# Kernel optimization log

Hardware: AMD Instinct MI355X
Metric: run time of the kernel (lower is better)

## Reference

```python
import jax, jax.numpy as jnp
import numpy as np

B, S, H, NH = 1, 4096, 768, 12
D = H // NH  # per-head dim = 64


def setup_inputs() -> dict:
    key = jax.random.key(0)
    ks = jax.random.split(key, 10)
    p = 0.02  # param scale
    return {
        "x": jax.random.normal(ks[0], (B, S, H), jnp.float32),
        "Wq": jax.random.normal(ks[1], (H, H), jnp.float32) * p,
        "bq": jax.random.normal(ks[2], (H,), jnp.float32) * p,
        "Wk": jax.random.normal(ks[3], (H, H), jnp.float32) * p,
        "bk": jax.random.normal(ks[4], (H,), jnp.float32) * p,
        "Wv": jax.random.normal(ks[5], (H, H), jnp.float32) * p,
        "bv": jax.random.normal(ks[6], (H,), jnp.float32) * p,
        "Wo": jax.random.normal(ks[7], (H, H), jnp.float32) * p,
        "bo": jax.random.normal(ks[8], (H,), jnp.float32) * p,
        "attn_mask": jax.random.randint(ks[9], (B, 1, 1, S), 0, 2).astype(bool),
    }


def _split_heads(t):
    # [B, S, H] -> [B, NH, S, D]
    return t.reshape(B, S, NH, D).transpose(0, 2, 1, 3)


def reference(x, Wq, bq, Wk, bk, Wv, bv, Wo, bo, attn_mask):
    q = _split_heads(x @ Wq.T + bq)
    k = _split_heads(x @ Wk.T + bk)
    v = _split_heads(x @ Wv.T + bv)
    scores = jnp.einsum('bhqd,bhkd->bhqk', q, k) / np.sqrt(D).astype(np.float32)
    scores = jnp.where(attn_mask, jnp.float32(-1e9), scores)
    attn = jax.nn.softmax(scores, axis=-1)
    ctx = jnp.einsum('bhqk,bhkd->bhqd', attn, v)
    ctx = ctx.transpose(0, 2, 1, 3).reshape(B, S, H)  # merge heads
    return ctx @ Wo.T + bo
```

## Files before the change

### kernel.cpp

```cpp
#include <hip/hip_runtime.h>
#include <stdint.h>

#define S_LEN 4096
#define HDIM  768
#define NHEAD 12
#define DHEAD 64

typedef _Float16 f16;
typedef __attribute__((ext_vector_type(8)))  _Float16 f16x8;
typedef __attribute__((ext_vector_type(4)))  _Float16 f16x4;
typedef __attribute__((ext_vector_type(4)))  float    f32x4;
typedef __attribute__((ext_vector_type(16))) float    f32x16;

typedef __attribute__((address_space(1))) void gv_t;
typedef __attribute__((address_space(3))) void lv_t;

__device__ __forceinline__ void async_copy16(const void* g, void* l) {
  __builtin_amdgcn_global_load_lds((gv_t*)g, (lv_t*)l, 16, 0, 0);
}

__device__ __forceinline__ float fast_exp2(float x) {
#if __has_builtin(__builtin_amdgcn_exp2f)
  return __builtin_amdgcn_exp2f(x);
#else
  return exp2f(x);
#endif
}

__device__ __forceinline__ int swz4(int row) { return (row ^ (row >> 2)) & 3; }

constexpr size_t OFF_META = 0;
constexpr size_t OFF_RIDX = 256;
constexpr size_t OFF_XB   = 65536;
constexpr size_t SZ_XB    = (size_t)S_LEN * HDIM * 2;
constexpr size_t OFF_WQKV = OFF_XB + SZ_XB;
constexpr size_t SZ_WQKV  = (size_t)3 * HDIM * HDIM * 2;
constexpr size_t OFF_WO   = OFF_WQKV + SZ_WQKV;
constexpr size_t SZ_WO    = (size_t)HDIM * HDIM * 2;
constexpr size_t OFF_Q    = OFF_WO + SZ_WO;
constexpr size_t SZ_HD    = (size_t)NHEAD * S_LEN * DHEAD * 2;
constexpr size_t OFF_K    = OFF_Q + SZ_HD;
constexpr size_t OFF_VT   = OFF_K + SZ_HD;
constexpr size_t OFF_PO   = OFF_VT + SZ_HD;

__global__ __launch_bounds__(256) void k_prep(const float* __restrict__ x,
                                              const float* __restrict__ wq,
                                              const float* __restrict__ wk,
                                              const float* __restrict__ wv,
                                              const float* __restrict__ wo,
                                              const int* __restrict__ mi,
                                              f16* __restrict__ dst,
                                              int* __restrict__ ridx,
                                              int* __restrict__ meta) {
  __shared__ int s_flag;
  __shared__ int s_cnt[256];
  const int b = blockIdx.x, tid = threadIdx.x;
  if (b < 5376) {
    int i = b * 256 + tid;
    const float* src; int off;
    if (i < 786432) { src = x; off = i; }
    else {
      int j = i - 786432;
      int w = j / 147456;
      off = j - w * 147456;
      src = (w == 0) ? wq : (w == 1) ? wk : (w == 2) ? wv : wo;
    }
    float4 v = ((const float4*)src)[off];
    f16x4 h;
    h[0] = (f16)v.x; h[1] = (f16)v.y; h[2] = (f16)v.z; h[3] = (f16)v.w;
    ((f16x4*)dst)[i] = h;
    return;
  }
  if (tid == 0) s_flag = 1;
  __syncthreads();
  int bad = 0;
  #pragma unroll
  for (int k = 0; k < 4; ++k) {
    int v = mi[k * 256 + tid];
    if (v != 0 && v != 1) bad = 1;
  }
  if (bad) atomicAnd(&s_flag, 0);
  __syncthreads();
  const int isInt = s_flag;
  const unsigned char* mu8 = (const unsigned char*)mi;
  int keep[16]; int cnt = 0;
  const int s0 = tid * 16;
  #pragma unroll
  for (int k = 0; k < 16; ++k) {
    int mval = isInt ? mi[s0 + k] : (int)mu8[s0 + k];
    keep[k] = (mval == 0) ? 1 : 0;
    cnt += keep[k];
    ridx[s0 + k] = 0;
  }
  s_cnt[tid] = cnt;
  __syncthreads();
  for (int off = 1; off < 256; off <<= 1) {
    int t = (tid >= off) ? s_cnt[tid - off] : 0;
    __syncthreads();
    s_cnt[tid] += t;
    __syncthreads();
  }
  int base = s_cnt[tid] - cnt;
  #pragma unroll
  for (int k = 0; k < 16; ++k) {
    if (keep[k]) { ridx[base] = s0 + k; ++base; }
  }
  if (tid == 255) meta[0] = s_cnt[255];
}

__global__ __launch_bounds__(256) void k_qkv(
    const f16* __restrict__ xb, const f16* __restrict__ wqkv,
    const float* __restrict__ bq, const float* __restrict__ bk, const float* __restrict__ bv,
    const int* __restrict__ ridx, const int* __restrict__ meta,
    f16* __restrict__ Qh, f16* __restrict__ Kc, f16* __restrict__ Vtc) {
  __shared__ __attribute__((aligned(16))) f16 lA[128 * 64];
  __shared__ __attribute__((aligned(16))) f16 lB[128 * 64];
  __shared__ __attribute__((aligned(16))) f16 lT[64 * 132];
  const int tid = threadIdx.x;
  const int wid = tid >> 6, lane = tid & 63;
  const int hf = lane >> 5, l31 = lane & 31;
  const int wm = wid >> 1, wn = wid & 1;
  const int tn = blockIdx.x;
  const int m0 = blockIdx.y * 128;
  const int mat = tn / 6;
  const int nb = (tn % 6) * 128;
  const int kc = meta[0];
  const int kcp = (kc + 63) & ~63;
  if (mat != 0 && m0 >= kc) return;
  const f16* wbase = wqkv + (size_t)mat * HDIM * HDIM;

  const int r8 = tid >> 3;
  const int slot = tid & 7;
  const int gs = slot ^ (r8 & 7);
  const f16* asrc[4];
  #pragma unroll
  for (int it = 0; it < 4; ++it) {
    int r = it * 32 + r8;
    if (mat == 0) {
      asrc[it] = xb + (size_t)(m0 + r) * HDIM;
    } else {
      int g = (m0 + r < kc) ? ridx[m0 + r] : 0;
      asrc[it] = xb + (size_t)g * HDIM;
    }
  }

  f32x16 acc[2][2] = {};

  for (int k0 = 0; k0 < HDIM; k0 += 64) {
    #pragma unroll
    for (int it = 0; it < 4; ++it) {
      int r = it * 32 + r8;
      async_copy16((const char*)(asrc[it] + k0) + gs * 16,
                   (char*)lA + (it * 256 + wid * 64) * 16);
      async_copy16((const char*)(wbase + (size_t)(nb + r) * HDIM + k0) + gs * 16,
                   (char*)lB + (it * 256 + wid * 64) * 16);
    }
    __syncthreads();
    #pragma unroll
    for (int kk = 0; kk < 4; ++kk) {
      f16x8 af[2], bf[2];
      #pragma unroll
      for (int mi = 0; mi < 2; ++mi) {
        int row = wm * 64 + mi * 32 + l31;
        af[mi] = *(const f16x8*)&lA[row * 64 + ((((kk << 1) | hf) ^ (row & 7)) * 8)];
      }
      #pragma unroll
      for (int ni = 0; ni < 2; ++ni) {
        int row = wn * 64 + ni * 32 + l31;
        bf[ni] = *(const f16x8*)&lB[row * 64 + ((((kk << 1) | hf) ^ (row & 7)) * 8)];
      }
      #pragma unroll
      for (int mi = 0; mi < 2; ++mi)
        #pragma unroll
        for (int ni = 0; ni < 2; ++ni)
          acc[mi][ni] = __builtin_amdgcn_mfma_f32_32x32x16_f16(af[mi], bf[ni], acc[mi][ni], 0, 0, 0);
    }
    __syncthreads();
  }

  if (mat == 2) {
    const float* bias = bv;
    #pragma unroll
    for (int pass = 0; pass < 2; ++pass) {
      __syncthreads();
      if (wn == pass) {
        #pragma unroll
        for (int ni = 0; ni < 2; ++ni) {
          const int n = nb + wn * 64 + ni * 32 + l31;
          const float bn = bias[n];
          const int dloc = ni * 32 + l31;
          #pragma unroll
          for (int mi = 0; mi < 2; ++mi) {
            #pragma unroll
            for (int rg = 0; rg < 4; ++rg) {
              const int sbase = wm * 64 + mi * 32 + 8 * rg + 4 * hf;
              f16x4 v4;
              #pragma unroll
              for (int j = 0; j < 4; ++j) {
                const int s = m0 + sbase + j;
                v4[j] = (s < kc) ? (f16)(acc[mi][ni][rg * 4 + j] + bn) : (f16)0.f;
              }
              *(f16x4*)&lT[dloc * 132 + sbase] = v4;
            }
          }
        }
      }
      __syncthreads();
      const int headg = (nb >> 6) + pass;
      for (int u2 = tid; u2 < 1024; u2 += 256) {
        const int d = u2 >> 4, p8 = u2 & 15;
        const int base16 = (p8 >> 1) * 16, half = p8 & 1;
        f16x4 lo = *(const f16x4*)&lT[d * 132 + base16 + half * 4];
        f16x4 hi = *(const f16x4*)&lT[d * 132 + base16 + 8 + half * 4];
        f16x8 o;
        o[0] = lo[0]; o[1] = lo[1]; o[2] = lo[2]; o[3] = lo[3];
        o[4] = hi[0]; o[5] = hi[1]; o[6] = hi[2]; o[7] = hi[3];
        *(f16x8*)&Vtc[((size_t)headg * DHEAD + d) * S_LEN + m0 + p8 * 8] = o;
      }
    }
    return;
  }

  const float* bias = (mat == 0) ? bq : bk;
  const float qscale = 0.125f * 1.44269504088896341f;
  #pragma unroll
  for (int mi = 0; mi < 2; ++mi) {
    #pragma unroll
    for (int ni = 0; ni < 2; ++ni) {
      int n = nb + wn * 64 + ni * 32 + l31;
      int head = n >> 6, d = n & 63;
      float b = bias[n];
      #pragma unroll
      for (int reg = 0; reg < 16; ++reg) {
        int s = m0 + wm * 64 + mi * 32 + (reg & 3) + 8 * (reg >> 2) + 4 * hf;
        float val = acc[mi][ni][reg] + b;
        if (mat == 0) {
          Qh[((size_t)head * S_LEN + s) * DHEAD + d] = (f16)(val * qscale);
        } else if (s < kc) {
          Kc[((size_t)head * S_LEN + s) * DHEAD + d] = (f16)val;
        } else if (s < kcp) {
          Kc[((size_t)head * S_LEN + s) * DHEAD + d] = (f16)0.f;
        }
      }
    }
  }
}

__global__ __launch_bounds__(128, 2) void k_attn(
    const f16* __restrict__ Qh, const f16* __restrict__ Kc, const f16* __restrict__ Vtc,
    const int* __restrict__ meta, f16* __restrict__ PO) {
  __shared__ __attribute__((aligned(16))) f16 lK[2][64 * 64];
  __shared__ __attribute__((aligned(16))) f16 lV[2][64 * 64];
  __shared__ float lil[64];
  const int tid = threadIdx.x;
  const int wid = tid >> 6, lane = tid & 63;
  const int hf = lane >> 5, l31 = lane & 31, r7 = l31 & 7;

  const int lid = blockIdx.x;
  const int w = ((lid & 7) * 96) + (lid >> 3);
  const int head = w >> 6;
  const int q0 = (w & 63) * 64 + wid * 32;

  const int kc = meta[0];
  const int nkt = (kc + 63) >> 6;

  const f16* Qp = Qh + ((size_t)head * S_LEN + q0 + l31) * DHEAD;
  f16x8 qf[4];
  #pragma unroll
  for (int dc = 0; dc < 4; ++dc) qf[dc] = *(const f16x8*)(Qp + dc * 16 + hf * 8);

  f32x16 accO[2] = {};
  float ls0 = 0.f, ls1 = 0.f, ls2 = 0.f, ls3 = 0.f;

  const char* kbase = (const char*)(Kc + (size_t)head * S_LEN * DHEAD);
  const char* vbase = (const char*)(Vtc + (size_t)head * DHEAD * S_LEN);

  const int crow = tid >> 3, cslot = tid & 7;
  const int gsc = cslot ^ (crow & 7);

  auto stage = [&](int t, int buf) {
    const int j0 = t * 64;
    #pragma unroll
    for (int it = 0; it < 4; ++it) {
      const int row = it * 16 + crow;
      async_copy16(kbase + (size_t)(j0 + row) * 128 + gsc * 16,
                   (char*)&lK[buf][0] + (it * 128 + wid * 64) * 16);
      async_copy16(vbase + (size_t)row * (S_LEN * 2) + (size_t)j0 * 2 + gsc * 16,
                   (char*)&lV[buf][0] + (it * 128 + wid * 64) * 16);
    }
  };

  int cur = 0;
  stage(0, 0);
  __syncthreads();

  for (int t = 0; t < nkt; ++t) {
    const bool more = (t + 1 < nkt);
    if (more) stage(t + 1, cur ^ 1);

    f16x8 af0[4], af1[4];
    #pragma unroll
    for (int dc = 0; dc < 4; ++dc) {
      af0[dc] = *(const f16x8*)&lK[cur][l31 * 64 + ((((dc << 1) | hf) ^ r7) * 8)];
      af1[dc] = *(const f16x8*)&lK[cur][(32 + l31) * 64 + ((((dc << 1) | hf) ^ r7) * 8)];
    }
    f32x16 sA = {}, sB = {};
    #pragma unroll
    for (int dc = 0; dc < 4; ++dc) {
      sA = __builtin_amdgcn_mfma_f32_32x32x16_f16(af0[dc], qf[dc], sA, 0, 0, 0);
      sB = __builtin_amdgcn_mfma_f32_32x32x16_f16(af1[dc], qf[dc], sB, 0, 0, 0);
    }

    f16x8 pfA[2];
    #pragma unroll
    for (int u = 0; u < 16; ++u) {
      sA[u] = fast_exp2(sA[u]);
      if (u & 1) ls1 += sA[u]; else ls0 += sA[u];
    }
    #pragma unroll
    for (int cc = 0; cc < 2; ++cc)
      #pragma unroll
      for (int u = 0; u < 8; ++u) pfA[cc][u] = (f16)sA[8 * cc + u];

    #pragma unroll
    for (int cc = 0; cc < 2; ++cc) {
      #pragma unroll
      for (int dh = 0; dh < 2; ++dh) {
        const int vrow = dh * 32 + l31;
        f16x8 vf = *(const f16x8*)&lV[cur][vrow * 64 + ((((cc << 1) | hf) ^ r7) * 8)];
        accO[dh] = __builtin_amdgcn_mfma_f32_32x32x16_f16(pfA[cc], vf, accO[dh], 0, 0, 0);
      }
    }

    f16x8 pfB[2];
    #pragma unroll
    for (int u = 0; u < 16; ++u) {
      sB[u] = fast_exp2(sB[u]);
      if (u & 1) ls3 += sB[u]; else ls2 += sB[u];
    }
    #pragma unroll
    for (int cc = 0; cc < 2; ++cc)
      #pragma unroll
      for (int u = 0; u < 8; ++u) pfB[cc][u] = (f16)sB[8 * cc + u];

    #pragma unroll
    for (int cc = 0; cc < 2; ++cc) {
      #pragma unroll
      for (int dh = 0; dh < 2; ++dh) {
        const int vrow = dh * 32 + l31;
        f16x8 vf = *(const f16x8*)&lV[cur][vrow * 64 + (((((2 + cc) << 1) | hf) ^ r7) * 8)];
        accO[dh] = __builtin_amdgcn_mfma_f32_32x32x16_f16(pfB[cc], vf, accO[dh], 0, 0, 0);
      }
    }

    if (more) {
      __syncthreads();
      cur ^= 1;
    }
  }

  float lsum = (ls0 + ls1) + (ls2 + ls3);
  lsum += __shfl_xor(lsum, 32);
  lsum -= (float)(nkt * 64 - kc);
  if (hf == 0) lil[wid * 32 + l31] = 1.0f / lsum;
  __syncthreads();

  f16* ost = (f16*)lK + wid * 2048;
  #pragma unroll
  for (int dh = 0; dh < 2; ++dh)
    #pragma unroll
    for (int reg = 0; reg < 16; ++reg) {
      int row = (reg & 3) + 8 * (reg >> 2) + 4 * hf;
      ost[row * 64 + dh * 32 + l31] = (f16)(accO[dh][reg] * lil[wid * 32 + row]);
    }
  #pragma unroll
  for (int p = 0; p < 4; ++p) {
    int row = p * 8 + (lane >> 3), sl = lane & 7;
    f16x8 v = *(const f16x8*)&ost[row * 64 + sl * 8];
    *(f16x8*)&PO[((size_t)head * S_LEN + q0 + row) * DHEAD + sl * 8] = v;
  }
}

__global__ __launch_bounds__(256) void k_out(
    const f16* __restrict__ PO, const f16* __restrict__ wo,
    const float* __restrict__ bo, float* __restrict__ out) {
  __shared__ __attribute__((aligned(16))) f16 lA[128 * 64];
  __shared__ __attribute__((aligned(16))) f16 lB[64 * 64];
  const int tid = threadIdx.x;
  const int wid = tid >> 6, lane = tid & 63;
  const int hf = lane >> 5, l31 = lane & 31;
  const int wm = wid >> 1, wn = wid & 1;
  const int lid = blockIdx.x;
  const int w = ((lid & 7) * 48) + (lid >> 3);
  const int nb = (w % 12) * 64;
  const int m0 = (w / 12) * 128;

  f32x16 acc[2] = {};

  for (int head = 0; head < NHEAD; ++head) {
    #pragma unroll
    for (int it = 0; it < 4; ++it) {
      int c = it * 256 + tid;
      int row = c >> 3, slot = c & 7;
      int gs = slot ^ (row & 7);
      async_copy16((const char*)(PO + ((size_t)head * S_LEN + m0 + row) * DHEAD) + gs * 16,
                   (char*)lA + (it * 256 + wid * 64) * 16);
    }
    #pragma unroll
    for (int it = 0; it < 2; ++it) {
      int c = it * 256 + tid;
      int row = c >> 3, slot = c & 7;
      int gs = slot ^ (row & 7);
      async_copy16((const char*)(wo + (size_t)(nb + row) * HDIM + head * 64) + gs * 16,
                   (char*)lB + (it * 256 + wid * 64) * 16);
    }
    __syncthreads();
    #pragma unroll
    for (int kk = 0; kk < 4; ++kk) {
      f16x8 af[2], bf;
      #pragma unroll
      for (int mi = 0; mi < 2; ++mi) {
        int row = wm * 64 + mi * 32 + l31;
        af[mi] = *(const f16x8*)&lA[row * 64 + ((((kk << 1) | hf) ^ (row & 7)) * 8)];
      }
      int rb = wn * 32 + l31;
      bf = *(const f16x8*)&lB[rb * 64 + ((((kk << 1) | hf) ^ (rb & 7)) * 8)];
      #pragma unroll
      for (int mi = 0; mi < 2; ++mi)
        acc[mi] = __builtin_amdgcn_mfma_f32_32x32x16_f16(af[mi], bf, acc[mi], 0, 0, 0);
    }
    __syncthreads();
  }

  const int n = nb + wn * 32 + l31;
  const float b = bo[n];
  #pragma unroll
  for (int mi = 0; mi < 2; ++mi) {
    #pragma unroll
    for (int reg = 0; reg < 16; ++reg) {
      int s = m0 + wm * 64 + mi * 32 + (reg & 3) + 8 * (reg >> 2) + 4 * hf;
      out[(size_t)s * HDIM + n] = acc[mi][reg] + b;
    }
  }
}

extern "C" void kernel_launch(void* const* d_in, const int* in_sizes, int n_in,
                              void* d_out, int out_size, void* d_ws, size_t ws_size,
                              hipStream_t stream) {
  const float* x  = (const float*)d_in[0];
  const float* Wq = (const float*)d_in[1];
  const float* bq = (const float*)d_in[2];
  const float* Wk = (const float*)d_in[3];
  const float* bk = (const float*)d_in[4];
  const float* Wv = (const float*)d_in[5];
  const float* bv = (const float*)d_in[6];
  const float* Wo = (const float*)d_in[7];
  const float* bo = (const float*)d_in[8];
  const int*   mask = (const int*)d_in[9];
  float* out = (float*)d_out;

  char* ws = (char*)d_ws;
  int* meta  = (int*)(ws + OFF_META);
  int* ridx  = (int*)(ws + OFF_RIDX);
  f16* xb    = (f16*)(ws + OFF_XB);
  f16* wqkv  = (f16*)(ws + OFF_WQKV);
  f16* wob   = (f16*)(ws + OFF_WO);
  f16* Qh    = (f16*)(ws + OFF_Q);
  f16* Kc    = (f16*)(ws + OFF_K);
  f16* Vtc   = (f16*)(ws + OFF_VT);
  f16* PO    = (f16*)(ws + OFF_PO);

  k_prep<<<dim3(5377), 256, 0, stream>>>(x, Wq, Wk, Wv, Wo, mask, xb, ridx, meta);
  k_qkv<<<dim3(18, 32), 256, 0, stream>>>(xb, wqkv, bq, bk, bv, ridx, meta, Qh, Kc, Vtc);
  k_attn<<<dim3(768), 128, 0, stream>>>(Qh, Kc, Vtc, meta, PO);
  k_out<<<dim3(384), 256, 0, stream>>>(PO, wob, bo, out);
}
```

Baseline: 168.0 us.

## Use single-wave attention blocks with barrier-free vmcnt-gated K/V prefetch pipeline

Attention blocks shrink from two waves to one, so each block handles 32 query rows and the grid doubles. Because only one wave touches LDS, __syncthreads is replaced by explicit vmcnt/lgkmcnt waits and sched barriers. K is double-buffered two tiles ahead while V is single-buffered and reloaded after its use. This removes block-wide barrier stalls and lets K loads overlap compute. In exchange, each wave issues twice the copy instructions, K/V tiles are no longer shared between waves so L2 traffic rises, and the hand-counted waitcnt values are fragile.

```diff
diff --git a/kernel.cpp b/kernel.cpp
--- a/kernel.cpp
+++ b/kernel.cpp
@@ -246,20 +246,19 @@
   }
 }
 
-__global__ __launch_bounds__(128, 2) void k_attn(
+__global__ __launch_bounds__(64, 2) void k_attn(
     const f16* __restrict__ Qh, const f16* __restrict__ Kc, const f16* __restrict__ Vtc,
     const int* __restrict__ meta, f16* __restrict__ PO) {
-  __shared__ __attribute__((aligned(16))) f16 lK[2][64 * 64];
-  __shared__ __attribute__((aligned(16))) f16 lV[2][64 * 64];
-  __shared__ float lil[64];
-  const int tid = threadIdx.x;
-  const int wid = tid >> 6, lane = tid & 63;
+  __shared__ __attribute__((aligned(16))) f16 kb[2][64 * 64];
+  __shared__ __attribute__((aligned(16))) f16 vb[64 * 64];
+  __shared__ float lil[32];
+  const int lane = threadIdx.x & 63;
   const int hf = lane >> 5, l31 = lane & 31, r7 = l31 & 7;
 
   const int lid = blockIdx.x;
-  const int w = ((lid & 7) * 96) + (lid >> 3);
-  const int head = w >> 6;
-  const int q0 = (w & 63) * 64 + wid * 32;
+  const int u = ((lid & 7) * 192) + (lid >> 3);
+  const int head = u >> 7;
+  const int q0 = (u & 127) * 32;
 
   const int kc = meta[0];
   const int nkt = (kc + 63) >> 6;
@@ -268,6 +267,8 @@
   f16x8 qf[4];
   #pragma unroll
   for (int dc = 0; dc < 4; ++dc) qf[dc] = *(const f16x8*)(Qp + dc * 16 + hf * 8);
+  asm volatile("s_waitcnt vmcnt(0)" ::: "memory");
+  __builtin_amdgcn_sched_barrier(0);
 
   f32x16 accO[2] = {};
   float ls0 = 0.f, ls1 = 0.f, ls2 = 0.f, ls3 = 0.f;
@@ -275,34 +276,45 @@
   const char* kbase = (const char*)(Kc + (size_t)head * S_LEN * DHEAD);
   const char* vbase = (const char*)(Vtc + (size_t)head * DHEAD * S_LEN);
 
-  const int crow = tid >> 3, cslot = tid & 7;
-  const int gsc = cslot ^ (crow & 7);
-
-  auto stage = [&](int t, int buf) {
+  const int r8l = lane >> 3, slot = lane & 7;
+  const int gsc = slot ^ (r8l & 7);
+
+  auto stageK = [&](int t, int buf) {
     const int j0 = t * 64;
     #pragma unroll
-    for (int it = 0; it < 4; ++it) {
-      const int row = it * 16 + crow;
+    for (int it = 0; it < 8; ++it) {
+      const int row = it * 8 + r8l;
       async_copy16(kbase + (size_t)(j0 + row) * 128 + gsc * 16,
-                   (char*)&lK[buf][0] + (it * 128 + wid * 64) * 16);
+                   (char*)&kb[buf][0] + it * 1024);
+    }
+  };
+  auto stageV = [&](int t) {
+    const int j0 = t * 64;
+    #pragma unroll
+    for (int it = 0; it < 8; ++it) {
+      const int row = it * 8 + r8l;
       async_copy16(vbase + (size_t)row * (S_LEN * 2) + (size_t)j0 * 2 + gsc * 16,
-                   (char*)&lV[buf][0] + (it * 128 + wid * 64) * 16);
+                   (char*)&vb[0] + it * 1024);
     }
   };
 
-  int cur = 0;
-  stage(0, 0);
-  __syncthreads();
+  stageK(0, 0);
+  stageV(0);
+  if (nkt > 1) stageK(1, 1);
 
   for (int t = 0; t < nkt; ++t) {
     const bool more = (t + 1 < nkt);
-    if (more) stage(t + 1, cur ^ 1);
+    const int cur = t & 1;
+
+    if (more) asm volatile("s_waitcnt vmcnt(16)" ::: "memory");
+    else      asm volatile("s_waitcnt vmcnt(8)"  ::: "memory");
+    __builtin_amdgcn_sched_barrier(0);
 
     f16x8 af0[4], af1[4];
     #pragma unroll
     for (int dc = 0; dc < 4; ++dc) {
-      af0[dc] = *(const f16x8*)&lK[cur][l31 * 64 + ((((dc << 1) | hf) ^ r7) * 8)];
-      af1[dc] = *(const f16x8*)&lK[cur][(32 + l31) * 64 + ((((dc << 1) | hf) ^ r7) * 8)];
+      af0[dc] = *(const f16x8*)&kb[cur][l31 * 64 + ((((dc << 1) | hf) ^ r7) * 8)];
+      af1[dc] = *(const f16x8*)&kb[cur][(32 + l31) * 64 + ((((dc << 1) | hf) ^ r7) * 8)];
     }
     f32x16 sA = {}, sB = {};
     #pragma unroll
@@ -313,65 +325,68 @@
 
     f16x8 pfA[2];
     #pragma unroll
-    for (int u = 0; u < 16; ++u) {
-      sA[u] = fast_exp2(sA[u]);
-      if (u & 1) ls1 += sA[u]; else ls0 += sA[u];
+    for (int uu = 0; uu < 16; ++uu) {
+      sA[uu] = fast_exp2(sA[uu]);
+      if (uu & 1) ls1 += sA[uu]; else ls0 += sA[uu];
     }
     #pragma unroll
     for (int cc = 0; cc < 2; ++cc)
       #pragma unroll
-      for (int u = 0; u < 8; ++u) pfA[cc][u] = (f16)sA[8 * cc + u];
+      for (int uu = 0; uu < 8; ++uu) pfA[cc][uu] = (f16)sA[8 * cc + uu];
+
+    if (more) asm volatile("s_waitcnt vmcnt(8)" ::: "memory");
+    else      asm volatile("s_waitcnt vmcnt(0)" ::: "memory");
+    __builtin_amdgcn_sched_barrier(0);
 
     #pragma unroll
     for (int cc = 0; cc < 2; ++cc) {
       #pragma unroll
       for (int dh = 0; dh < 2; ++dh) {
         const int vrow = dh * 32 + l31;
-        f16x8 vf = *(const f16x8*)&lV[cur][vrow * 64 + ((((cc << 1) | hf) ^ r7) * 8)];
+        f16x8 vf = *(const f16x8*)&vb[vrow * 64 + ((((cc << 1) | hf) ^ r7) * 8)];
         accO[dh] = __builtin_amdgcn_mfma_f32_32x32x16_f16(pfA[cc], vf, accO[dh], 0, 0, 0);
       }
     }
 
     f16x8 pfB[2];
     #pragma unroll
-    for (int u = 0; u < 16; ++u) {
-      sB[u] = fast_exp2(sB[u]);
-      if (u & 1) ls3 += sB[u]; else ls2 += sB[u];
+    for (int uu = 0; uu < 16; ++uu) {
+      sB[uu] = fast_exp2(sB[uu]);
+      if (uu & 1) ls3 += sB[uu]; else ls2 += sB[uu];
     }
     #pragma unroll
     for (int cc = 0; cc < 2; ++cc)
       #pragma unroll
-      for (int u = 0; u < 8; ++u) pfB[cc][u] = (f16)sB[8 * cc + u];
+      for (int uu = 0; uu < 8; ++uu) pfB[cc][uu] = (f16)sB[8 * cc + uu];
 
     #pragma unroll
     for (int cc = 0; cc < 2; ++cc) {
       #pragma unroll
       for (int dh = 0; dh < 2; ++dh) {
         const int vrow = dh * 32 + l31;
-        f16x8 vf = *(const f16x8*)&lV[cur][vrow * 64 + (((((2 + cc) << 1) | hf) ^ r7) * 8)];
+        f16x8 vf = *(const f16x8*)&vb[vrow * 64 + (((((2 + cc) << 1) | hf) ^ r7) * 8)];
         accO[dh] = __builtin_amdgcn_mfma_f32_32x32x16_f16(pfB[cc], vf, accO[dh], 0, 0, 0);
       }
     }
 
-    if (more) {
-      __syncthreads();
-      cur ^= 1;
-    }
+    asm volatile("s_waitcnt lgkmcnt(0)" ::: "memory");
+    __builtin_amdgcn_sched_barrier(0);
+    if (more) stageV(t + 1);
+    if (t + 2 < nkt) stageK(t + 2, cur);
   }
 
   float lsum = (ls0 + ls1) + (ls2 + ls3);
   lsum += __shfl_xor(lsum, 32);
   lsum -= (float)(nkt * 64 - kc);
-  if (hf == 0) lil[wid * 32 + l31] = 1.0f / lsum;
-  __syncthreads();
-
-  f16* ost = (f16*)lK + wid * 2048;
+  if (hf == 0) lil[l31] = 1.0f / lsum;
+
+  f16* ost = (f16*)kb;
   #pragma unroll
   for (int dh = 0; dh < 2; ++dh)
     #pragma unroll
     for (int reg = 0; reg < 16; ++reg) {
       int row = (reg & 3) + 8 * (reg >> 2) + 4 * hf;
-      ost[row * 64 + dh * 32 + l31] = (f16)(accO[dh][reg] * lil[wid * 32 + row]);
+      ost[row * 64 + dh * 32 + l31] = (f16)(accO[dh][reg] * lil[row]);
     }
   #pragma unroll
   for (int p = 0; p < 4; ++p) {
@@ -472,6 +487,6 @@
 
   k_prep<<<dim3(5377), 256, 0, stream>>>(x, Wq, Wk, Wv, Wo, mask, xb, ridx, meta);
   k_qkv<<<dim3(18, 32), 256, 0, stream>>>(xb, wqkv, bq, bk, bv, ridx, meta, Qh, Kc, Vtc);
-  k_attn<<<dim3(768), 128, 0, stream>>>(Qh, Kc, Vtc, meta, PO);
+  k_attn<<<dim3(1536), 64, 0, stream>>>(Qh, Kc, Vtc, meta, PO);
   k_out<<<dim3(384), 256, 0, stream>>>(PO, wob, bo, out);
 }
```

Result: no change. 169.6 us (+0.9%).
